# Optimization experiments

Hardware: AMD Instinct MI355X
Metric: run time of the kernel (lower is better)

## Reference

```python
import jax, jax.numpy as jnp
import numpy as np

B, D, TX, TY = 32, 192, 256, 1024
NEG = -1e9


def setup_inputs() -> dict:
    key = jax.random.key(0)
    k1, k2, k3, k4 = jax.random.split(key, 4)
    x = jax.random.normal(k1, (B, D, TX), jnp.float32)
    y = jax.random.normal(k2, (B, D, TY), jnp.float32)
    # ensure 1 <= x_lens <= TX <= y_lens <= TY so a monotonic path exists
    x_lens = jax.random.randint(k3, (B,), 64, TX + 1, jnp.int32)
    y_lens = jax.random.randint(k4, (B,), 512, TY + 1, jnp.int32)
    return {"x": x, "x_lens": x_lens, "y": y, "y_lens": y_lens}


def _log_prior(x, y):
    # Gaussian log-prior: factor = -0.5 everywhere, so
    # log_prior[b,t,s] = -0.5*sum_d y^2 + sum_d x*y - 0.5*sum_d x^2 + const
    ndim = x.shape[1]
    const = jnp.asarray(-0.5 * np.log(2.0 * np.pi) * ndim, x.dtype)
    y_sq = -0.5 * jnp.sum(y * y, axis=1)            # [B, TY]
    x_sq = -0.5 * jnp.sum(x * x, axis=1)            # [B, TX]
    xy = jnp.einsum('bdt,bds->bts', x, y)           # [B, TX, TY]
    return y_sq[:, None, :] + xy + x_sq[:, :, None] + const


def _maximum_path(log_prior, x_lens, y_lens):
    # Viterbi-style monotonic alignment search (Glow-TTS / VITS maximum_path).
    b, tx, ty = log_prior.shape
    xr = jnp.arange(tx)

    # --- forward DP over mel frames (columns of the (tx, ty) grid) ---
    col0 = jnp.where(xr[None, :] == 0, log_prior[:, :, 0], NEG)  # [B, TX]

    def fwd(prev, inp):
        lp_col, yi = inp                               # lp_col: [B, TX]
        v_cur = jnp.where(xr[None, :] == yi, NEG, prev)
        v_prev = jnp.concatenate(
            [jnp.full((b, 1), NEG, prev.dtype), prev[:, :-1]], axis=1)
        cur = lp_col + jnp.maximum(v_cur, v_prev)
        return cur, cur

    lp_t = jnp.moveaxis(log_prior, 2, 0)               # [TY, B, TX]
    _, cols = jax.lax.scan(fwd, col0, (lp_t[1:], jnp.arange(1, ty)))
    value = jnp.concatenate([col0[None], cols], axis=0)  # [TY, B, TX]

    # value at column y-1 (dummy at y=0, never used for the decision there)
    vprev = jnp.concatenate([value[:1], value[:-1]], axis=0)

    # --- backtrack from (x_lens-1, y_lens-1) down to y=0 ---
    def bwd(index, inp):
        yi, vpc = inp                                  # vpc: [B, TX]
        active = yi < y_lens                           # [B]
        row = jnp.where(active[:, None],
                        jax.nn.one_hot(index, tx, dtype=log_prior.dtype), 0.0)
        vm1 = jnp.take_along_axis(
            vpc, jnp.maximum(index - 1, 0)[:, None], axis=1)[:, 0]
        v0 = jnp.take_along_axis(vpc, index[:, None], axis=1)[:, 0]
        move = (index != 0) & ((index == yi) | (vm1 > v0)) & active
        return index - move.astype(index.dtype), row

    idx0 = x_lens - 1
    _, rows = jax.lax.scan(bwd, idx0, (jnp.arange(ty), vprev), reverse=True)
    return jnp.moveaxis(rows, 0, 2)                    # [B, TX, TY]


def reference(x, x_lens, y, y_lens):
    log_prior = _log_prior(x, y)
    attn = _maximum_path(log_prior, x_lens, y_lens)
    return jax.lax.stop_gradient(attn)
```

## Files before the change

kernel.cpp:

```cpp
#include <hip/hip_runtime.h>
#include <stdint.h>

#define B_  32
#define D_  192
#define TX_ 256
#define TY_ 1024
#define NEGV -1e9f
#define LPCONST ((float)(-176.43619837529715))

__global__ __launch_bounds__(256) void k0_sq(const float* __restrict__ x,
                                             const float* __restrict__ y,
                                             float* __restrict__ xsq,
                                             float* __restrict__ ysq) {
    int gid = blockIdx.x * 256 + threadIdx.x;
    if (gid < B_ * TX_) {
        int b = gid >> 8, t = gid & 255;
        const float* p = x + (size_t)b * D_ * TX_ + t;
        float s = 0.f;
        #pragma unroll 8
        for (int d = 0; d < D_; ++d) { float v = p[(size_t)d * TX_]; s += v * v; }
        xsq[gid] = -0.5f * s;
    } else {
        int g = gid - B_ * TX_;
        int b = g >> 10, t = g & 1023;
        const float* p = y + (size_t)b * D_ * TY_ + t;
        float s = 0.f;
        #pragma unroll 8
        for (int d = 0; d < D_; ++d) { float v = p[(size_t)d * TY_]; s += v * v; }
        ysq[g] = -0.5f * s;
    }
}

#define BT 128
#define BS 128
#define BK 32
__global__ __launch_bounds__(256) void k1_gemm(const float* __restrict__ x,
                                               const float* __restrict__ y,
                                               const float* __restrict__ xsq,
                                               const float* __restrict__ ysq,
                                               float* __restrict__ lp) {
    __shared__ float xs[BK][BT];
    __shared__ float ys[BK][BS];
    const int id = blockIdx.x;
    const int r  = id & 7;
    const int g  = id >> 3;
    const int b  = r + 8 * (g >> 4);
    const int sub = g & 15;
    const int t0 = (sub >> 3) * BT;
    const int s0 = (sub & 7) * BS;
    const int tid = threadIdx.x;
    const int ti = tid & 15;
    const int si = tid >> 4;

    float acc[8][8];
    #pragma unroll
    for (int i = 0; i < 8; ++i)
        #pragma unroll
        for (int j = 0; j < 8; ++j) acc[i][j] = 0.f;

    const float* xg = x + (size_t)b * D_ * TX_ + t0;
    const float* yg = y + (size_t)b * D_ * TY_ + s0;

    for (int k0 = 0; k0 < D_; k0 += BK) {
        #pragma unroll
        for (int i = 0; i < 4; ++i) {
            int f = tid + i * 256;
            int row = f >> 5;
            int col = (f & 31) * 4;
            float4 v = *(const float4*)(xg + (size_t)(k0 + row) * TX_ + col);
            *(float4*)&xs[row][col] = v;
            float4 w = *(const float4*)(yg + (size_t)(k0 + row) * TY_ + col);
            *(float4*)&ys[row][col] = w;
        }
        __syncthreads();
        #pragma unroll
        for (int k = 0; k < BK; ++k) {
            float xr[8], yr[8];
            *(float4*)&xr[0] = *(float4*)&xs[k][ti * 8];
            *(float4*)&xr[4] = *(float4*)&xs[k][ti * 8 + 4];
            *(float4*)&yr[0] = *(float4*)&ys[k][si * 8];
            *(float4*)&yr[4] = *(float4*)&ys[k][si * 8 + 4];
            #pragma unroll
            for (int i = 0; i < 8; ++i)
                #pragma unroll
                for (int j = 0; j < 8; ++j) acc[i][j] += xr[i] * yr[j];
        }
        __syncthreads();
    }

    float xq[8], yq[8];
    *(float4*)&xq[0] = *(const float4*)(xsq + b * TX_ + t0 + ti * 8);
    *(float4*)&xq[4] = *(const float4*)(xsq + b * TX_ + t0 + ti * 8 + 4);
    *(float4*)&yq[0] = *(const float4*)(ysq + b * TY_ + s0 + si * 8);
    *(float4*)&yq[4] = *(const float4*)(ysq + b * TY_ + s0 + si * 8 + 4);

    #pragma unroll
    for (int js = 0; js < 8; ++js) {
        float* op = lp + (size_t)(b * TY_ + s0 + si * 8 + js) * TX_ + t0 + ti * 8;
        float o[8];
        #pragma unroll
        for (int it = 0; it < 8; ++it) {
            float v = yq[js] + acc[it][js];
            v = v + xq[it];
            o[it] = v + LPCONST;
        }
        *(float4*)op       = *(float4*)&o[0];
        *(float4*)(op + 4) = *(float4*)&o[4];
    }
}

__device__ __forceinline__ void gload16(const float* gp, float* lp_) {
    __builtin_amdgcn_global_load_lds(
        (const __attribute__((address_space(1))) unsigned int*)(gp),
        (__attribute__((address_space(3))) unsigned int*)(lp_), 16, 0, 0);
}

__global__ __launch_bounds__(256, 1) void k2_dp(const float* __restrict__ lp,
                                                const int* __restrict__ xlens,
                                                const int* __restrict__ ylens,
                                                unsigned char* __restrict__ path) {
    __shared__ float colbuf[2][32 * 256];
    __shared__ unsigned int RB[TX_][33];
    __shared__ unsigned int PTw[TY_ / 4];
    unsigned char* PT = (unsigned char*)PTw;

    const int b   = blockIdx.x;
    const int tid = threadIdx.x;
    const int w   = tid >> 6;
    const int l   = tid & 63;
    const int xlen = xlens[b];
    const int ylen = ylens[b];
    const int nchunk = (ylen + 31) >> 5;
    const float* lpb = lp + (size_t)b * TY_ * TX_;
    const int tt0 = l * 4;
    const int l4  = l * 4;

#define LOADCHUNK(kc, bufI) {                                           \
    for (int c = w - 1; c < 32; c += 3) {                               \
        int sg = (kc) * 32 + c; if (sg > TY_ - 1) sg = TY_ - 1;         \
        gload16(lpb + (size_t)sg * TX_ + l4, &colbuf[bufI][c * 256]);   \
    }                                                                   \
}

#define COLRD(bufI, j) (*(float4*)&colbuf[bufI][(j) * 256 + l4])

#define PROC2(sv, sbitv, fv, PRE) {                                     \
    bool e0 = false, e1 = false, e2 = false, e3 = false;                \
    if (PRE) { e0 = (tt0 == (sv));     e1 = (tt0 + 1 == (sv));          \
               e2 = (tt0 + 2 == (sv)); e3 = (tt0 + 3 == (sv)); }        \
    if ((l != 0) && (e0 || (shv > p0))) rw0 |= (sbitv);                 \
    if (e1 || (p0 > p1)) rw1 |= (sbitv);                                \
    if (e2 || (p1 > p2)) rw2 |= (sbitv);                                \
    if (e3 || (p2 > p3)) rw3 |= (sbitv);                                \
    float c3 = (fv).w + fmaxf(e3 ? NEGV : p3, p2);                      \
    float nsh = __shfl_up(c3, 1);                                       \
    float c2 = (fv).z + fmaxf(e2 ? NEGV : p2, p1);                      \
    float c1 = (fv).y + fmaxf(e1 ? NEGV : p1, p0);                      \
    float c0 = (fv).x + fmaxf(e0 ? NEGV : p0, (l == 0) ? NEGV : shv);   \
    p0 = c0; p1 = c1; p2 = c2; p3 = c3; shv = nsh;                      \
}

#define FLUSH(wd) { RB[tt0][wd] = rw0; RB[tt0 + 1][wd] = rw1;           \
                    RB[tt0 + 2][wd] = rw2; RB[tt0 + 3][wd] = rw3;       \
                    rw0 = rw1 = rw2 = rw3 = 0; }

    float4 rr[8];
    float p0, p1, p2, p3, shv;
    unsigned int rw0 = 0, rw1 = 0, rw2 = 0, rw3 = 0;

    if (w > 0) LOADCHUNK(0, 0)
    __syncthreads();

    for (int k = 0; k < nchunk; ++k) {
        const int cb = k & 1;
        if (w > 0) {
            if (k + 1 < nchunk) {
                if (w == 1) LOADCHUNK(k + 1, cb ^ 1)
                else if (w == 2) LOADCHUNK(k + 1, cb ^ 1)
                else LOADCHUNK(k + 1, cb ^ 1)
            }
        } else {
            #pragma unroll
            for (int j = 0; j < 8; ++j) rr[j] = COLRD(cb, j);
            if (k == 0) {
                p0 = (l == 0) ? rr[0].x : NEGV;
                p1 = NEGV; p2 = NEGV; p3 = NEGV;
                shv = NEGV;
                rr[0] = COLRD(0, 8);
                #pragma unroll
                for (int j = 1; j < 32; ++j) {
                    PROC2(j, 1u << j, rr[j & 7], true)
                    if (j < 24) rr[j & 7] = COLRD(0, j + 8);
                }
            } else if (k < 8) {
                const int s0c = k << 5;
                #pragma unroll
                for (int j = 0; j < 32; ++j) {
                    PROC2(s0c + j, 1u << j, rr[j & 7], true)
                    if (j < 24) rr[j & 7] = COLRD(cb, j + 8);
                }
            } else {
                #pragma unroll
                for (int j = 0; j < 32; ++j) {
                    PROC2(0, 1u << j, rr[j & 7], false)
                    if (j < 24) rr[j & 7] = COLRD(cb, j + 8);
                }
            }
            FLUSH(k)
        }
        __syncthreads();
    }

    if (tid == 0) {
        int idx = xlen - 1;
        int yi = ylen - 1;
        int wd = yi >> 5;
        unsigned int cur = RB[idx][wd];
        unsigned int below = (idx > 0) ? RB[idx - 1][wd] : 0u;
        while (yi >= 0) {
            unsigned int m = cur & (0xFFFFFFFFu >> (31 - (yi & 31)));
            if (m) {
                int hb = 31 - __clz(m);
                int lo = (wd << 5) + hb;
                for (int q = lo; q <= yi; ++q) PT[q] = (unsigned char)idx;
                --idx;
                cur = below;
                below = (idx > 0) ? RB[idx - 1][wd] : 0u;
                yi = lo - 1;
                if (yi >= 0 && (yi >> 5) < wd) {
                    wd = yi >> 5;
                    cur = RB[idx][wd];
                    below = (idx > 0) ? RB[idx - 1][wd] : 0u;
                }
            } else {
                int lo = wd << 5;
                for (int q = lo; q <= yi; ++q) PT[q] = (unsigned char)idx;
                yi = lo - 1;
                if (yi >= 0) {
                    --wd;
                    cur = RB[idx][wd];
                    below = (idx > 0) ? RB[idx - 1][wd] : 0u;
                }
            }
        }
    }
    __syncthreads();
    ((unsigned int*)(path + b * TY_))[tid] = PTw[tid];
}

__global__ __launch_bounds__(256) void k3_out(const unsigned char* __restrict__ path,
                                              const int* __restrict__ ylens,
                                              float* __restrict__ out) {
    int F = blockIdx.x * 256 + threadIdx.x;
    int yi = (F & 255) * 4;
    int t  = (F >> 8) & 255;
    int b  = F >> 16;
    int ylen = ylens[b];
    unsigned int pw = *(const unsigned int*)(path + b * TY_ + yi);
    float4 v;
    v.x = (((pw      ) & 255u) == (unsigned)t && yi     < ylen) ? 1.f : 0.f;
    v.y = (((pw >>  8) & 255u) == (unsigned)t && yi + 1 < ylen) ? 1.f : 0.f;
    v.z = (((pw >> 16) & 255u) == (unsigned)t && yi + 2 < ylen) ? 1.f : 0.f;
    v.w = (((pw >> 24) & 255u) == (unsigned)t && yi + 3 < ylen) ? 1.f : 0.f;
    ((float4*)out)[F] = v;
}

extern "C" void kernel_launch(void* const* d_in, const int* in_sizes, int n_in,
                              void* d_out, int out_size, void* d_ws, size_t ws_size,
                              hipStream_t stream) {
    const float* x  = (const float*)d_in[0];
    const int*   xl = (const int*)d_in[1];
    const float* y  = (const float*)d_in[2];
    const int*   yl = (const int*)d_in[3];
    float* out = (float*)d_out;

    char* ws = (char*)d_ws;
    float* xsq = (float*)ws;
    float* ysq = (float*)(ws + 32 * 1024);
    unsigned char* path = (unsigned char*)(ws + 160 * 1024);

    float* lp = out;

    k0_sq  <<<160, 256, 0, stream>>>(x, y, xsq, ysq);
    k1_gemm<<<512, 256, 0, stream>>>(x, y, xsq, ysq, lp);
    k2_dp  <<<B_, 256, 0, stream>>>(lp, xl, yl, path);
    k3_out <<<(B_ * TX_ * TY_ / 4) / 256, 256, 0, stream>>>(path, yl, out);
}
```

Before: 187.0 us.

## Pipeline DP across four wavefronts with one row per lane and DPP shifts

The DP kernel no longer uses one compute wave with three loader waves staging columns into LDS. Now all four wavefronts compute, each owning 64 rows (one row per lane), in a wavefront pipeline skewed by one 32-column group per wave. Boundary values pass between waves through a small LDS ring, and neighbour shifts within a wave use DPP row_shr. Each lane loads its log-prior values straight from global memory into registers, prefetching the next group, which drops the LDS staging. This adds pipeline fill and drain steps and a barrier per group, and relies on strided scalar global loads.

```diff
diff --git a/kernel.cpp b/kernel.cpp
--- a/kernel.cpp
+++ b/kernel.cpp
@@ -109,104 +109,78 @@
     }
 }
 
-__device__ __forceinline__ void gload16(const float* gp, float* lp_) {
-    __builtin_amdgcn_global_load_lds(
-        (const __attribute__((address_space(1))) unsigned int*)(gp),
-        (__attribute__((address_space(3))) unsigned int*)(lp_), 16, 0, 0);
+__device__ __forceinline__ float wshr1(float v) {
+    int r = __builtin_amdgcn_update_dpp(0, __float_as_int(v),
+                                        0x138, 0xF, 0xF, false);
+    return __int_as_float(r);
 }
 
 __global__ __launch_bounds__(256, 1) void k2_dp(const float* __restrict__ lp,
                                                 const int* __restrict__ xlens,
                                                 const int* __restrict__ ylens,
                                                 unsigned char* __restrict__ path) {
-    __shared__ float colbuf[2][32 * 256];
     __shared__ unsigned int RB[TX_][33];
     __shared__ unsigned int PTw[TY_ / 4];
+    __shared__ float bnd[4][128];
     unsigned char* PT = (unsigned char*)PTw;
 
-    const int b   = blockIdx.x;
     const int tid = threadIdx.x;
     const int w   = tid >> 6;
     const int l   = tid & 63;
+    const int b   = blockIdx.x;
     const int xlen = xlens[b];
     const int ylen = ylens[b];
-    const int nchunk = (ylen + 31) >> 5;
-    const float* lpb = lp + (size_t)b * TY_ * TX_;
-    const int tt0 = l * 4;
-    const int l4  = l * 4;
-
-#define LOADCHUNK(kc, bufI) {                                           \
-    for (int c = w - 1; c < 32; c += 3) {                               \
-        int sg = (kc) * 32 + c; if (sg > TY_ - 1) sg = TY_ - 1;         \
-        gload16(lpb + (size_t)sg * TX_ + l4, &colbuf[bufI][c * 256]);   \
-    }                                                                   \
-}
-
-#define COLRD(bufI, j) (*(float4*)&colbuf[bufI][(j) * 256 + l4])
-
-#define PROC2(sv, sbitv, fv, PRE) {                                     \
-    bool e0 = false, e1 = false, e2 = false, e3 = false;                \
-    if (PRE) { e0 = (tt0 == (sv));     e1 = (tt0 + 1 == (sv));          \
-               e2 = (tt0 + 2 == (sv)); e3 = (tt0 + 3 == (sv)); }        \
-    if ((l != 0) && (e0 || (shv > p0))) rw0 |= (sbitv);                 \
-    if (e1 || (p0 > p1)) rw1 |= (sbitv);                                \
-    if (e2 || (p1 > p2)) rw2 |= (sbitv);                                \
-    if (e3 || (p2 > p3)) rw3 |= (sbitv);                                \
-    float c3 = (fv).w + fmaxf(e3 ? NEGV : p3, p2);                      \
-    float nsh = __shfl_up(c3, 1);                                       \
-    float c2 = (fv).z + fmaxf(e2 ? NEGV : p2, p1);                      \
-    float c1 = (fv).y + fmaxf(e1 ? NEGV : p1, p0);                      \
-    float c0 = (fv).x + fmaxf(e0 ? NEGV : p0, (l == 0) ? NEGV : shv);   \
-    p0 = c0; p1 = c1; p2 = c2; p3 = c3; shv = nsh;                      \
-}
-
-#define FLUSH(wd) { RB[tt0][wd] = rw0; RB[tt0 + 1][wd] = rw1;           \
-                    RB[tt0 + 2][wd] = rw2; RB[tt0 + 3][wd] = rw3;       \
-                    rw0 = rw1 = rw2 = rw3 = 0; }
-
-    float4 rr[8];
-    float p0, p1, p2, p3, shv;
-    unsigned int rw0 = 0, rw1 = 0, rw2 = 0, rw3 = 0;
-
-    if (w > 0) LOADCHUNK(0, 0)
-    __syncthreads();
-
-    for (int k = 0; k < nchunk; ++k) {
-        const int cb = k & 1;
-        if (w > 0) {
-            if (k + 1 < nchunk) {
-                if (w == 1) LOADCHUNK(k + 1, cb ^ 1)
-                else if (w == 2) LOADCHUNK(k + 1, cb ^ 1)
-                else LOADCHUNK(k + 1, cb ^ 1)
-            }
-        } else {
-            #pragma unroll
-            for (int j = 0; j < 8; ++j) rr[j] = COLRD(cb, j);
-            if (k == 0) {
-                p0 = (l == 0) ? rr[0].x : NEGV;
-                p1 = NEGV; p2 = NEGV; p3 = NEGV;
-                shv = NEGV;
-                rr[0] = COLRD(0, 8);
+    const int send = (ylen + 31) & ~31;
+    const int groups = send >> 5;
+    const int row  = (w << 6) + l;
+    const int rowc = (row < xlen) ? row : (xlen - 1);
+    const float* base = lp + (size_t)b * TY_ * TX_ + rowc;
+    const bool isL0  = (l == 0);
+    const bool tzero = (row == 0);
+    const bool pub   = (w < 3) && (l == 63);
+
+    float r[32];
+    #pragma unroll
+    for (int j = 0; j < 32; ++j) r[j] = base[(size_t)j * TX_];
+
+    float v = NEGV;
+    unsigned int rw = 0;
+
+    #pragma unroll 1
+    for (int p = 0; p < groups + 3; ++p) {
+        const int k = p - w;
+        if (k >= 0 && k < groups) {
+            const int c = k << 5;
+            const bool PREg = ((k >> 1) == w);
+            float bv[32];
+            if (w > 0) {
+                const float* bp = bnd[w - 1];
                 #pragma unroll
-                for (int j = 1; j < 32; ++j) {
-                    PROC2(j, 1u << j, rr[j & 7], true)
-                    if (j < 24) rr[j & 7] = COLRD(0, j + 8);
-                }
-            } else if (k < 8) {
-                const int s0c = k << 5;
-                #pragma unroll
-                for (int j = 0; j < 32; ++j) {
-                    PROC2(s0c + j, 1u << j, rr[j & 7], true)
-                    if (j < 24) rr[j & 7] = COLRD(cb, j + 8);
-                }
+                for (int j = 0; j < 32; ++j) bv[j] = bp[(c - 1 + j) & 127];
             } else {
                 #pragma unroll
-                for (int j = 0; j < 32; ++j) {
-                    PROC2(0, 1u << j, rr[j & 7], false)
-                    if (j < 24) rr[j & 7] = COLRD(cb, j + 8);
+                for (int j = 0; j < 32; ++j) bv[j] = NEGV;
+            }
+            #pragma unroll
+            for (int j = 0; j < 32; ++j) {
+                const int sC = c + j;
+                if (j == 0 && k == 0) {
+                    v = tzero ? r[0] : NEGV;
+                } else {
+                    float a = wshr1(v);
+                    float below = isL0 ? bv[j] : a;
+                    bool e = PREg && (row == sC);
+                    bool mv = (!tzero) && (e || (below > v));
+                    if (mv) rw |= (1u << j);
+                    float vc = e ? NEGV : v;
+                    float vp = tzero ? NEGV : below;
+                    v = r[j] + fmaxf(vc, vp);
                 }
+                if (pub) bnd[w][sC & 127] = v;
+                int cc = sC + 32; if (cc > TY_ - 1) cc = TY_ - 1;
+                r[j] = base[(size_t)cc * TX_];
             }
-            FLUSH(k)
+            RB[row][k] = rw; rw = 0;
         }
         __syncthreads();
     }
```

Result: slower. 198.0 us (+5.9%).
